# Kernel tuning notes

Hardware: AMD Instinct MI355X
Metric: run time of the kernel (lower is better)

## Reference

```python
import jax, jax.numpy as jnp
import numpy as np

N_NODES = 50000
N_EDGES = 400000
D_IN = 512
DIM_H = 256
N_GRAPHS = 64
BN_EPS = 1e-5


def _linear_init(key, din, dout):
    kw, kb = jax.random.split(key)
    s = 1.0 / np.sqrt(din)
    W = jax.random.uniform(kw, (din, dout), jnp.float32, -s, s)
    b = jax.random.uniform(kb, (dout,), jnp.float32, -s, s)
    return W, b


def setup_inputs() -> dict:
    key = jax.random.key(0)
    ks = iter(jax.random.split(key, 64))
    inp = {}
    inp["x"] = jax.random.normal(next(ks), (N_NODES, D_IN), jnp.float32)
    inp["edge_index"] = jax.random.randint(next(ks), (2, N_EDGES), 0, N_NODES, jnp.int32)
    inp["batch"] = jnp.sort(jax.random.randint(next(ks), (N_NODES,), 0, N_GRAPHS, jnp.int32))
    dins = [D_IN, DIM_H, DIM_H]
    for l in range(3):
        p = "c%d_" % (l + 1)
        inp[p + "W1"], inp[p + "b1"] = _linear_init(next(ks), dins[l], DIM_H)
        inp[p + "gamma"] = jax.random.uniform(next(ks), (DIM_H,), jnp.float32, 0.5, 1.5)
        inp[p + "beta"] = 0.1 * jax.random.normal(next(ks), (DIM_H,), jnp.float32)
        inp[p + "mean"] = 0.1 * jax.random.normal(next(ks), (DIM_H,), jnp.float32)
        inp[p + "var"] = jax.random.uniform(next(ks), (DIM_H,), jnp.float32, 0.5, 1.5)
        inp[p + "W2"], inp[p + "b2"] = _linear_init(next(ks), DIM_H, DIM_H)
    inp["lin1_W"], inp["lin1_b"] = _linear_init(next(ks), 3 * DIM_H, 64)
    inp["lin2_W"], inp["lin2_b"] = _linear_init(next(ks), 64, 2)
    return inp


def _gin_layer(x, src, dst, W1, b1, gamma, beta, mean, var, W2, b2):
    # GINConv with eps=0: h_i = MLP(x_i + sum_{j->i} x_j); scatter-add over edges
    agg = jax.ops.segment_sum(x[src], dst, num_segments=x.shape[0])
    h = (x + agg) @ W1 + b1
    # eval-mode BatchNorm1d
    h = jax.nn.relu((h - mean) * jax.lax.rsqrt(var + BN_EPS) * gamma + beta)
    return jax.nn.relu(h @ W2 + b2)


def reference(x, edge_index, batch,
              c1_W1, c1_b1, c1_gamma, c1_beta, c1_mean, c1_var, c1_W2, c1_b2,
              c2_W1, c2_b1, c2_gamma, c2_beta, c2_mean, c2_var, c2_W2, c2_b2,
              c3_W1, c3_b1, c3_gamma, c3_beta, c3_mean, c3_var, c3_W2, c3_b2,
              lin1_W, lin1_b, lin2_W, lin2_b):
    src, dst = edge_index[0], edge_index[1]
    h1 = _gin_layer(x, src, dst, c1_W1, c1_b1, c1_gamma, c1_beta, c1_mean, c1_var, c1_W2, c1_b2)
    h2 = _gin_layer(h1, src, dst, c2_W1, c2_b1, c2_gamma, c2_beta, c2_mean, c2_var, c2_W2, c2_b2)
    h3 = _gin_layer(h2, src, dst, c3_W1, c3_b1, c3_gamma, c3_beta, c3_mean, c3_var, c3_W2, c3_b2)
    # global_add_pool per graph
    p1 = jax.ops.segment_sum(h1, batch, num_segments=N_GRAPHS)
    p2 = jax.ops.segment_sum(h2, batch, num_segments=N_GRAPHS)
    p3 = jax.ops.segment_sum(h3, batch, num_segments=N_GRAPHS)
    h = jnp.concatenate([p1, p2, p3], axis=1)
    h = jax.nn.relu(h @ lin1_W + lin1_b)
    # Dropout(p=0.8) is identity in eval mode
    h = h @ lin2_W + lin2_b
    return (h, jax.nn.log_softmax(h, axis=1))
```

## Files before the change

kernel.cpp:

```cpp
#include <hip/hip_runtime.h>
#include <hip/hip_bf16.h>

#define DIV_UP(a,b) (((a)+(b)-1)/(b))

static const int NN  = 50000;
static const int NE  = 400000;
static const int DIN = 512;
static const int DH  = 256;
static const int NG  = 64;
static const int MAXDEG = 64;

typedef unsigned short u16;
typedef unsigned int   u32;
typedef __attribute__((ext_vector_type(8))) short bf16x8;
typedef __attribute__((ext_vector_type(4))) float f32x4;

#define AS1(p) ((const __attribute__((address_space(1))) void*)(p))
#define AS3(p) ((__attribute__((address_space(3))) void*)(p))

__device__ inline u16 f2bf(float f) {
  u32 u = __float_as_uint(f);
  u += 0x7fffu + ((u >> 16) & 1u);
  return (u16)(u >> 16);
}
__device__ inline float bf2f(u16 h) { return __uint_as_float(((u32)h) << 16); }
__device__ inline void unpack2(u32 u, float& lo, float& hi) {
  lo = __uint_as_float(u << 16);
  hi = __uint_as_float(u & 0xffff0000u);
}
__device__ inline u32 pack2(float lo, float hi) {
  return (u32)f2bf(lo) | ((u32)f2bf(hi) << 16);
}

struct SetupArgs {
  const float* x; u16* Xb;
  const float* Wsrc[6]; u16* Wdst[6];
  const float* bn[15];
  float* scsh;
  int* cnt; float* PL;
};
static const int NB_X = (NN * DIN / 8) / 256;
static const int NB_W = (131072 + 5 * 65536) / 256;
static const int NB_Z = DIV_UP(NN + NG * 768, 256);

__global__ __launch_bounds__(256) void k_setup(SetupArgs a) {
  int b = blockIdx.x;
  if (b < NB_X) {
    int i = b * 256 + threadIdx.x;
    const float4* p = (const float4*)a.x + (size_t)i * 2;
    float4 f0 = p[0], f1 = p[1];
    uint4 o;
    o.x = pack2(f0.x, f0.y); o.y = pack2(f0.z, f0.w);
    o.z = pack2(f1.x, f1.y); o.w = pack2(f1.z, f1.w);
    ((uint4*)a.Xb)[i] = o;
  } else if (b < NB_X + NB_W) {
    int idx = (b - NB_X) * 256 + threadIdx.x;
    if (idx < 131072) {
      int n = idx >> 9, k = idx & 511;
      a.Wdst[0][idx] = f2bf(a.Wsrc[0][(size_t)k * 256 + n]);
    } else {
      int r = idx - 131072;
      int s = 1 + (r >> 16);
      int ri = r & 65535;
      int n = ri >> 8, k = ri & 255;
      a.Wdst[s][ri] = f2bf(a.Wsrc[s][(size_t)k * 256 + n]);
    }
  } else if (b < NB_X + NB_W + 3) {
    int l = b - NB_X - NB_W, ch = threadIdx.x;
    float sc = rsqrtf(a.bn[l * 5 + 4][ch] + 1e-5f) * a.bn[l * 5 + 1][ch];
    float sh = (a.bn[l * 5 + 0][ch] - a.bn[l * 5 + 3][ch]) * sc + a.bn[l * 5 + 2][ch];
    a.scsh[l * 512 + ch] = sc;
    a.scsh[l * 512 + 256 + ch] = sh;
  } else {
    int i = (b - NB_X - NB_W - 3) * 256 + threadIdx.x;
    if (i < NN) a.cnt[i] = 0;
    else if (i - NN < NG * 768) a.PL[i - NN] = 0.f;
  }
}

__global__ __launch_bounds__(256) void k_fill2(const int* __restrict__ src,
                                               const int* __restrict__ dst,
                                               int* __restrict__ cnt,
                                               int* __restrict__ adj, int nE) {
  int e = blockIdx.x * 256 + threadIdx.x;
  if (e >= nE) return;
  int d = dst[e];
  int pos = atomicAdd(&cnt[d], 1);
  if (pos < MAXDEG) adj[(size_t)d * MAXDEG + pos] = src[e];
}

__global__ __launch_bounds__(256) void k_gather_bn(const u16* __restrict__ Y,
                                                   const int* __restrict__ cnt,
                                                   const int* __restrict__ adj,
                                                   const float* __restrict__ scsh,
                                                   u16* __restrict__ A) {
  int gid = blockIdx.x * 256 + threadIdx.x;
  int i = gid >> 5;
  if (i >= NN) return;
  int c = (gid & 31) << 3;
  uint4 v = *(const uint4*)(Y + (size_t)i * DH + c);
  float a0,a1,a2,a3,a4,a5,a6,a7;
  unpack2(v.x,a0,a1); unpack2(v.y,a2,a3); unpack2(v.z,a4,a5); unpack2(v.w,a6,a7);
  int deg = cnt[i]; if (deg > MAXDEG) deg = MAXDEG;
  const int* row = adj + (size_t)i * MAXDEG;
  int e = 0;
  for (; e + 8 <= deg; e += 8) {
    uint4 w[8];
#pragma unroll
    for (int u = 0; u < 8; ++u)
      w[u] = *(const uint4*)(Y + (size_t)row[e + u] * DH + c);
#pragma unroll
    for (int u = 0; u < 8; ++u) {
      float b0,b1,b2,b3,b4,b5,b6,b7;
      unpack2(w[u].x,b0,b1); unpack2(w[u].y,b2,b3);
      unpack2(w[u].z,b4,b5); unpack2(w[u].w,b6,b7);
      a0+=b0; a1+=b1; a2+=b2; a3+=b3; a4+=b4; a5+=b5; a6+=b6; a7+=b7;
    }
  }
  for (; e + 4 <= deg; e += 4) {
    uint4 w[4];
#pragma unroll
    for (int u = 0; u < 4; ++u)
      w[u] = *(const uint4*)(Y + (size_t)row[e + u] * DH + c);
#pragma unroll
    for (int u = 0; u < 4; ++u) {
      float b0,b1,b2,b3,b4,b5,b6,b7;
      unpack2(w[u].x,b0,b1); unpack2(w[u].y,b2,b3);
      unpack2(w[u].z,b4,b5); unpack2(w[u].w,b6,b7);
      a0+=b0; a1+=b1; a2+=b2; a3+=b3; a4+=b4; a5+=b5; a6+=b6; a7+=b7;
    }
  }
  for (; e < deg; ++e) {
    uint4 w = *(const uint4*)(Y + (size_t)row[e] * DH + c);
    float b0,b1,b2,b3,b4,b5,b6,b7;
    unpack2(w.x,b0,b1); unpack2(w.y,b2,b3); unpack2(w.z,b4,b5); unpack2(w.w,b6,b7);
    a0+=b0; a1+=b1; a2+=b2; a3+=b3; a4+=b4; a5+=b5; a6+=b6; a7+=b7;
  }
  float4 sc0 = *(const float4*)(scsh + c);
  float4 sc1 = *(const float4*)(scsh + c + 4);
  float4 sh0 = *(const float4*)(scsh + 256 + c);
  float4 sh1 = *(const float4*)(scsh + 256 + c + 4);
  a0 = fmaxf(fmaf(a0, sc0.x, sh0.x), 0.f);
  a1 = fmaxf(fmaf(a1, sc0.y, sh0.y), 0.f);
  a2 = fmaxf(fmaf(a2, sc0.z, sh0.z), 0.f);
  a3 = fmaxf(fmaf(a3, sc0.w, sh0.w), 0.f);
  a4 = fmaxf(fmaf(a4, sc1.x, sh1.x), 0.f);
  a5 = fmaxf(fmaf(a5, sc1.y, sh1.y), 0.f);
  a6 = fmaxf(fmaf(a6, sc1.z, sh1.z), 0.f);
  a7 = fmaxf(fmaf(a7, sc1.w, sh1.w), 0.f);
  uint4 o;
  o.x = pack2(a0,a1); o.y = pack2(a2,a3); o.z = pack2(a4,a5); o.w = pack2(a6,a7);
  *(uint4*)(A + (size_t)i * DH + c) = o;
}

template <int MODE, int POOL, int STORE, int K>
__global__ __launch_bounds__(256) void k_gemm_mfma(
    const u16* __restrict__ A, const u16* __restrict__ BT,
    const float* __restrict__ bias, u16* __restrict__ out,
    const int* __restrict__ batch, float* __restrict__ PL, int poolOff, int M) {
  const int N = 256;
  __shared__ __align__(16) u16 sm[4 * 128 * 64];
  __shared__ int bsh[128];
  u16* Cs = sm;
  const int bm = blockIdx.x * 128;
  const int bn = blockIdx.y * 128;
  const int tid = threadIdx.x;
  const int lane = tid & 63;
  const int wave = tid >> 6;
  const int wm = (wave >> 1) * 64;
  const int wn = (wave & 1) * 64;
  const int l15 = lane & 15;
  const int l4 = lane >> 4;
  const int lrow = lane >> 3;
  const int lcol = (lane & 7) * 8;

  if (POOL && tid < 128) {
    int gm = bm + tid;
    bsh[tid] = (gm < M) ? batch[gm] : -1;
  }

  auto STAGE = [&](int buf, int k0) {
    u16* As = sm + buf * 2 * 128 * 64;
    u16* Bs = As + 128 * 64;
#pragma unroll
    for (int i = 0; i < 4; ++i) {
      int q = wave * 4 + i;
      int row = q * 8 + lrow;
      int grA = bm + row; if (grA >= M) grA = M - 1;
      __builtin_amdgcn_global_load_lds(AS1(A + (size_t)grA * K + k0 + lcol),
                                       AS3(As + q * 512), 16, 0, 0);
      __builtin_amdgcn_global_load_lds(AS1(BT + (size_t)(bn + row) * K + k0 + lcol),
                                       AS3(Bs + q * 512), 16, 0, 0);
    }
  };

  f32x4 acc[4][4] = {};
  const int nt = K >> 6;
  STAGE(0, 0);
  int cur = 0;
  for (int t = 0; t < nt; ++t) {
    __syncthreads();
    if (t + 1 < nt) STAGE(cur ^ 1, (t + 1) << 6);
    u16* As = sm + cur * 2 * 128 * 64;
    u16* Bs = As + 128 * 64;
#pragma unroll
    for (int ks = 0; ks < 2; ++ks) {
      bf16x8 af[4], bf_[4];
#pragma unroll
      for (int f = 0; f < 4; ++f) {
        af[f]  = *(const bf16x8*)(As + (wm + f * 16 + l15) * 64 + ks * 32 + l4 * 8);
        bf_[f] = *(const bf16x8*)(Bs + (wn + f * 16 + l15) * 64 + ks * 32 + l4 * 8);
      }
#pragma unroll
      for (int i = 0; i < 4; ++i)
#pragma unroll
        for (int j = 0; j < 4; ++j)
          acc[i][j] = __builtin_amdgcn_mfma_f32_16x16x32_bf16(af[i], bf_[j], acc[i][j], 0, 0, 0);
    }
    cur ^= 1;
  }

  __syncthreads();
#pragma unroll
  for (int j = 0; j < 4; ++j) {
    int n = bn + wn + j * 16 + l15;
    float sh = (MODE == 1) ? bias[n] : 0.f;
#pragma unroll
    for (int i = 0; i < 4; ++i) {
#pragma unroll
      for (int r = 0; r < 4; ++r) {
        int row = wm + i * 16 + l4 * 4 + r;
        int col = wn + j * 16 + l15;
        float v = acc[i][j][r] + sh;
        if (MODE == 1) v = fmaxf(v, 0.f);
        Cs[row * 128 + col] = f2bf(v);
      }
    }
  }
  __syncthreads();

  if (STORE) {
    const int ccol = (tid & 15) * 8;
#pragma unroll
    for (int p = 0; p < 8; ++p) {
      int row = p * 16 + (tid >> 4);
      int gm = bm + row;
      if (gm < M)
        *(uint4*)(out + (size_t)gm * N + bn + ccol) =
            *(const uint4*)(Cs + row * 128 + ccol);
    }
  }

  if (POOL) {
    int col = tid & 127;
    int half = tid >> 7;
    float accv = 0.f;
    int cg = bsh[half * 64];
    for (int r = 0; r < 64; ++r) {
      int row = half * 64 + r;
      int g = bsh[row];
      if (g != cg) {
        if (cg >= 0) unsafeAtomicAdd(&PL[cg * 768 + poolOff + bn + col], accv);
        accv = 0.f;
        cg = g;
      }
      accv += bf2f(Cs[row * 128 + col]);
    }
    if (cg >= 0) unsafeAtomicAdd(&PL[cg * 768 + poolOff + bn + col], accv);
  }
}

__global__ __launch_bounds__(64) void k_head1(const float* __restrict__ P,
                                              const float* __restrict__ W,
                                              const float* __restrict__ b,
                                              float* __restrict__ Q) {
  __shared__ float pr[768];
  int g = blockIdx.x, t = threadIdx.x;
  for (int i = t; i < 768; i += 64) pr[i] = P[g * 768 + i];
  __syncthreads();
  float acc = b[t];
  for (int k = 0; k < 768; ++k) acc = fmaf(pr[k], W[k * 64 + t], acc);
  Q[g * 64 + t] = fmaxf(acc, 0.f);
}

__global__ __launch_bounds__(64) void k_head2(const float* __restrict__ Q,
                                              const float* __restrict__ W,
                                              const float* __restrict__ b,
                                              float* __restrict__ out) {
  int g = threadIdx.x;
  if (g >= 64) return;
  float h0 = b[0], h1 = b[1];
  for (int k = 0; k < 64; ++k) {
    float q = Q[g * 64 + k];
    h0 = fmaf(q, W[k * 2 + 0], h0);
    h1 = fmaf(q, W[k * 2 + 1], h1);
  }
  out[g * 2 + 0] = h0;
  out[g * 2 + 1] = h1;
  float m = fmaxf(h0, h1);
  float lse = m + logf(expf(h0 - m) + expf(h1 - m));
  out[128 + g * 2 + 0] = h0 - lse;
  out[128 + g * 2 + 1] = h1 - lse;
}

extern "C" void kernel_launch(void* const* d_in, const int* in_sizes, int n_in,
                              void* d_out, int out_size, void* d_ws,
                              size_t ws_size, hipStream_t stream) {
  const float* x = (const float*)d_in[0];
  const int* ei = (const int*)d_in[1];
  const int* batch = (const int*)d_in[2];
  const float* W1[3]; const float* b1[3]; const float* ga[3]; const float* be[3];
  const float* mu[3]; const float* va[3]; const float* W2[3]; const float* b2[3];
  for (int l = 0; l < 3; ++l) {
    int base = 3 + 8 * l;
    W1[l] = (const float*)d_in[base + 0];
    b1[l] = (const float*)d_in[base + 1];
    ga[l] = (const float*)d_in[base + 2];
    be[l] = (const float*)d_in[base + 3];
    mu[l] = (const float*)d_in[base + 4];
    va[l] = (const float*)d_in[base + 5];
    W2[l] = (const float*)d_in[base + 6];
    b2[l] = (const float*)d_in[base + 7];
  }
  const float* l1W = (const float*)d_in[27];
  const float* l1b = (const float*)d_in[28];
  const float* l2W = (const float*)d_in[29];
  const float* l2b = (const float*)d_in[30];
  const int* src = ei;
  const int* dst = ei + NE;
  float* out = (float*)d_out;

  char* w = (char*)d_ws;
  u16* Xb  = (u16*)w; w += (size_t)NN * DIN * 2;
  u16* Yb  = (u16*)w; w += (size_t)NN * DH * 2;
  u16* Ab  = (u16*)w; w += (size_t)NN * DH * 2;
  u16* H1b = (u16*)w; w += (size_t)NN * DH * 2;
  u16* H2b = (u16*)w; w += (size_t)NN * DH * 2;
  u16* W1T[3]; u16* W2T[3];
  W1T[0] = (u16*)w; w += (size_t)DIN * DH * 2;
  for (int l = 1; l < 3; ++l) { W1T[l] = (u16*)w; w += (size_t)DH * DH * 2; }
  for (int l = 0; l < 3; ++l) { W2T[l] = (u16*)w; w += (size_t)DH * DH * 2; }
  float* scsh = (float*)w; w += 3 * 512 * 4;
  float* PL = (float*)w; w += NG * 768 * 4;
  float* Q  = (float*)w; w += NG * 64 * 4;
  int* cnt  = (int*)w; w += (size_t)NN * 4;
  int* adj  = (int*)w; w += (size_t)NN * MAXDEG * 4;

  SetupArgs sa;
  sa.x = x; sa.Xb = Xb;
  sa.Wsrc[0] = W1[0]; sa.Wdst[0] = W1T[0];
  sa.Wsrc[1] = W1[1]; sa.Wdst[1] = W1T[1];
  sa.Wsrc[2] = W1[2]; sa.Wdst[2] = W1T[2];
  for (int l = 0; l < 3; ++l) { sa.Wsrc[3 + l] = W2[l]; sa.Wdst[3 + l] = W2T[l]; }
  for (int l = 0; l < 3; ++l) {
    sa.bn[l * 5 + 0] = b1[l]; sa.bn[l * 5 + 1] = ga[l]; sa.bn[l * 5 + 2] = be[l];
    sa.bn[l * 5 + 3] = mu[l]; sa.bn[l * 5 + 4] = va[l];
  }
  sa.scsh = scsh; sa.cnt = cnt; sa.PL = PL;
  k_setup<<<NB_X + NB_W + 3 + NB_Z, 256, 0, stream>>>(sa);

  k_fill2<<<DIV_UP(NE, 256), 256, 0, stream>>>(src, dst, cnt, adj, NE);

  dim3 gg(DIV_UP(NN, 128), 2);
  const u16* hin[3] = {Xb, H1b, H2b};
  u16* hout[3] = {H1b, H2b, H1b};

  for (int l = 0; l < 3; ++l) {
    if (l == 0)
      k_gemm_mfma<2, 0, 1, 512><<<gg, 256, 0, stream>>>(hin[l], W1T[l], nullptr, Yb,
                                                        nullptr, nullptr, 0, NN);
    else
      k_gemm_mfma<2, 0, 1, 256><<<gg, 256, 0, stream>>>(hin[l], W1T[l], nullptr, Yb,
                                                        nullptr, nullptr, 0, NN);
    k_gather_bn<<<DIV_UP(NN * 32, 256), 256, 0, stream>>>(Yb, cnt, adj,
                                                          scsh + l * 512, Ab);
    if (l < 2)
      k_gemm_mfma<1, 1, 1, 256><<<gg, 256, 0, stream>>>(Ab, W2T[l], b2[l], hout[l],
                                                        batch, PL, 256 * l, NN);
    else
      k_gemm_mfma<1, 1, 0, 256><<<gg, 256, 0, stream>>>(Ab, W2T[l], b2[l], hout[l],
                                                        batch, PL, 256 * l, NN);
  }

  k_head1<<<NG, 64, 0, stream>>>(PL, l1W, l1b, Q);
  k_head2<<<1, 64, 0, stream>>>(Q, l2W, l2b, out);
}
```

Measured before the change: 329.1 us.

## Widen GEMM tile to full 256 columns with 512-thread blocks and k-step 32

The MFMA GEMM now computes a 128x256 output tile per block using 8 waves, in place of two 128x128 blocks along N. The A tile is loaded once per block rather than twice, and the pooling epilogue covers all 256 columns with fewer atomics per row group. The K step drops from 64 to 32, which doubles the number of barrier-separated iterations. LDS layout and launch bounds change to match.

Result: faster. 287.9 us (-12.5%).

```diff
diff --git a/kernel.cpp b/kernel.cpp
--- a/kernel.cpp
+++ b/kernel.cpp
@@ -154,25 +154,24 @@
 }
 
 template <int MODE, int POOL, int STORE, int K>
-__global__ __launch_bounds__(256) void k_gemm_mfma(
+__global__ __launch_bounds__(512, 4) void k_gemm_mfma(
     const u16* __restrict__ A, const u16* __restrict__ BT,
     const float* __restrict__ bias, u16* __restrict__ out,
     const int* __restrict__ batch, float* __restrict__ PL, int poolOff, int M) {
   const int N = 256;
-  __shared__ __align__(16) u16 sm[4 * 128 * 64];
+  __shared__ __align__(16) u16 sm[32768];
   __shared__ int bsh[128];
   u16* Cs = sm;
   const int bm = blockIdx.x * 128;
-  const int bn = blockIdx.y * 128;
   const int tid = threadIdx.x;
   const int lane = tid & 63;
   const int wave = tid >> 6;
-  const int wm = (wave >> 1) * 64;
-  const int wn = (wave & 1) * 64;
+  const int wm = (wave >> 2) * 64;
+  const int wn = (wave & 3) * 64;
   const int l15 = lane & 15;
   const int l4 = lane >> 4;
-  const int lrow = lane >> 3;
-  const int lcol = (lane & 7) * 8;
+  const int srow = lane >> 2;
+  const int scol = (lane & 3) * 8;
 
   if (POOL && tid < 128) {
     int gm = bm + tid;
@@ -180,93 +179,92 @@
   }
 
   auto STAGE = [&](int buf, int k0) {
-    u16* As = sm + buf * 2 * 128 * 64;
-    u16* Bs = As + 128 * 64;
-#pragma unroll
-    for (int i = 0; i < 4; ++i) {
-      int q = wave * 4 + i;
-      int row = q * 8 + lrow;
+    u16* As = sm + buf * 12288;
+    u16* Bs = As + 4096;
+    {
+      int row = wave * 16 + srow;
       int grA = bm + row; if (grA >= M) grA = M - 1;
-      __builtin_amdgcn_global_load_lds(AS1(A + (size_t)grA * K + k0 + lcol),
-                                       AS3(As + q * 512), 16, 0, 0);
-      __builtin_amdgcn_global_load_lds(AS1(BT + (size_t)(bn + row) * K + k0 + lcol),
+      __builtin_amdgcn_global_load_lds(AS1(A + (size_t)grA * K + k0 + scol),
+                                       AS3(As + wave * 512), 16, 0, 0);
+    }
+#pragma unroll
+    for (int i = 0; i < 2; ++i) {
+      int q = wave * 2 + i;
+      int row = q * 16 + srow;
+      __builtin_amdgcn_global_load_lds(AS1(BT + (size_t)row * K + k0 + scol),
                                        AS3(Bs + q * 512), 16, 0, 0);
     }
   };
 
   f32x4 acc[4][4] = {};
-  const int nt = K >> 6;
+  const int nt = K >> 5;
   STAGE(0, 0);
   int cur = 0;
   for (int t = 0; t < nt; ++t) {
     __syncthreads();
-    if (t + 1 < nt) STAGE(cur ^ 1, (t + 1) << 6);
-    u16* As = sm + cur * 2 * 128 * 64;
-    u16* Bs = As + 128 * 64;
-#pragma unroll
-    for (int ks = 0; ks < 2; ++ks) {
-      bf16x8 af[4], bf_[4];
-#pragma unroll
-      for (int f = 0; f < 4; ++f) {
-        af[f]  = *(const bf16x8*)(As + (wm + f * 16 + l15) * 64 + ks * 32 + l4 * 8);
-        bf_[f] = *(const bf16x8*)(Bs + (wn + f * 16 + l15) * 64 + ks * 32 + l4 * 8);
-      }
-#pragma unroll
-      for (int i = 0; i < 4; ++i)
-#pragma unroll
-        for (int j = 0; j < 4; ++j)
-          acc[i][j] = __builtin_amdgcn_mfma_f32_16x16x32_bf16(af[i], bf_[j], acc[i][j], 0, 0, 0);
-    }
+    if (t + 1 < nt) STAGE(cur ^ 1, (t + 1) << 5);
+    u16* As = sm + cur * 12288;
+    u16* Bs = As + 4096;
+    bf16x8 af[4], bf_[4];
+#pragma unroll
+    for (int f = 0; f < 4; ++f) {
+      af[f]  = *(const bf16x8*)(As + (wm + f * 16 + l15) * 32 + l4 * 8);
+      bf_[f] = *(const bf16x8*)(Bs + (wn + f * 16 + l15) * 32 + l4 * 8);
+    }
+#pragma unroll
+    for (int i = 0; i < 4; ++i)
+#pragma unroll
+      for (int j = 0; j < 4; ++j)
+        acc[i][j] = __builtin_amdgcn_mfma_f32_16x16x32_bf16(af[i], bf_[j], acc[i][j], 0, 0, 0);
     cur ^= 1;
   }
 
   __syncthreads();
 #pragma unroll
   for (int j = 0; j < 4; ++j) {
-    int n = bn + wn + j * 16 + l15;
+    int n = wn + j * 16 + l15;
     float sh = (MODE == 1) ? bias[n] : 0.f;
 #pragma unroll
     for (int i = 0; i < 4; ++i) {
 #pragma unroll
       for (int r = 0; r < 4; ++r) {
         int row = wm + i * 16 + l4 * 4 + r;
-        int col = wn + j * 16 + l15;
         float v = acc[i][j][r] + sh;
         if (MODE == 1) v = fmaxf(v, 0.f);
-        Cs[row * 128 + col] = f2bf(v);
+        Cs[row * 256 + n] = f2bf(v);
       }
     }
   }
   __syncthreads();
 
   if (STORE) {
-    const int ccol = (tid & 15) * 8;
+    const int ccol = (tid & 31) * 8;
 #pragma unroll
     for (int p = 0; p < 8; ++p) {
-      int row = p * 16 + (tid >> 4);
+      int row = p * 16 + (tid >> 5);
       int gm = bm + row;
       if (gm < M)
-        *(uint4*)(out + (size_t)gm * N + bn + ccol) =
-            *(const uint4*)(Cs + row * 128 + ccol);
+        *(uint4*)(out + (size_t)gm * N + ccol) =
+            *(const uint4*)(Cs + row * 256 + ccol);
     }
   }
 
   if (POOL) {
-    int col = tid & 127;
-    int half = tid >> 7;
+    int col = tid & 255;
+    int half = tid >> 8;
     float accv = 0.f;
     int cg = bsh[half * 64];
     for (int r = 0; r < 64; ++r) {
       int row = half * 64 + r;
       int g = bsh[row];
       if (g != cg) {
-        if (cg >= 0) unsafeAtomicAdd(&PL[cg * 768 + poolOff + bn + col], accv);
+        if (cg >= 0) unsafeAtomicAdd(&PL[cg * 768 + poolOff + col], accv);
         accv = 0.f;
         cg = g;
       }
-      accv += bf2f(Cs[row * 128 + col]);
-    }
-    if (cg >= 0) unsafeAtomicAdd(&PL[cg * 768 + poolOff + bn + col], accv);
+      accv += bf2f(Cs[row * 256 + col]);
+    }
+    if (cg >= 0) unsafeAtomicAdd(&PL[cg * 768 + poolOff + col], accv);
   }
 }
 
@@ -361,24 +359,24 @@
 
   k_fill2<<<DIV_UP(NE, 256), 256, 0, stream>>>(src, dst, cnt, adj, NE);
 
-  dim3 gg(DIV_UP(NN, 128), 2);
+  const int gg = DIV_UP(NN, 128);
   const u16* hin[3] = {Xb, H1b, H2b};
   u16* hout[3] = {H1b, H2b, H1b};
 
   for (int l = 0; l < 3; ++l) {
     if (l == 0)
-      k_gemm_mfma<2, 0, 1, 512><<<gg, 256, 0, stream>>>(hin[l], W1T[l], nullptr, Yb,
+      k_gemm_mfma<2, 0, 1, 512><<<gg, 512, 0, stream>>>(hin[l], W1T[l], nullptr, Yb,
                                                         nullptr, nullptr, 0, NN);
     else
-      k_gemm_mfma<2, 0, 1, 256><<<gg, 256, 0, stream>>>(hin[l], W1T[l], nullptr, Yb,
+      k_gemm_mfma<2, 0, 1, 256><<<gg, 512, 0, stream>>>(hin[l], W1T[l], nullptr, Yb,
                                                         nullptr, nullptr, 0, NN);
     k_gather_bn<<<DIV_UP(NN * 32, 256), 256, 0, stream>>>(Yb, cnt, adj,
                                                           scsh + l * 512, Ab);
     if (l < 2)
-      k_gemm_mfma<1, 1, 1, 256><<<gg, 256, 0, stream>>>(Ab, W2T[l], b2[l], hout[l],
+      k_gemm_mfma<1, 1, 1, 256><<<gg, 512, 0, stream>>>(Ab, W2T[l], b2[l], hout[l],
                                                         batch, PL, 256 * l, NN);
     else
-      k_gemm_mfma<1, 1, 0, 256><<<gg, 256, 0, stream>>>(Ab, W2T[l], b2[l], hout[l],
+      k_gemm_mfma<1, 1, 0, 256><<<gg, 512, 0, stream>>>(Ab, W2T[l], b2[l], hout[l],
                                                         batch, PL, 256 * l, NN);
   }
 
```
